# Performance work log

Hardware: AMD Instinct MI355X
Metric: run time of the kernel (lower is better)

## Reference

```python
import jax, jax.numpy as jnp
import numpy as np
import math

D_MODEL = 512
NUM_HEADS = 8
MAX_LEN = 10000.0


def positional_encoding_2d(seq_len, d_model, H, W, dtype=jnp.float32):
    # position along height repeated across width, and vice versa
    pos_h = jnp.repeat(jnp.arange(H, dtype=dtype), W)  # [H*W]
    pos_w = jnp.tile(jnp.arange(W, dtype=dtype), H)    # [H*W]
    div_term = jnp.exp(jnp.arange(0, d_model, 2, dtype=dtype) * (-(math.log(MAX_LEN) / d_model)))
    div = div_term[: d_model // 4]  # [d_model//4]
    pe = jnp.zeros((seq_len, d_model), dtype=dtype)
    pe = pe.at[:, 0::4].set(jnp.sin(pos_h[:, None] * div))
    pe = pe.at[:, 1::4].set(jnp.cos(pos_h[:, None] * div))
    pe = pe.at[:, 2::4].set(jnp.sin(pos_w[:, None] * div))
    pe = pe.at[:, 3::4].set(jnp.cos(pos_w[:, None] * div))
    return pe


def setup_inputs() -> dict:
    key = jax.random.key(0)
    ks = jax.random.split(key, 6)
    B, C, H, W = 8, D_MODEL, 32, 32
    d = D_MODEL
    s = 1.0 / math.sqrt(d)
    x = jax.random.normal(ks[0], (B, C, H, W), dtype=jnp.float32)
    Wq = jax.random.normal(ks[1], (d, d), dtype=jnp.float32) * s
    Wk = jax.random.normal(ks[2], (d, d), dtype=jnp.float32) * s
    Wv = jax.random.normal(ks[3], (d, d), dtype=jnp.float32) * s
    Wo = jax.random.normal(ks[4], (d, d), dtype=jnp.float32) * s
    bo = jnp.zeros((d,), dtype=jnp.float32)
    gamma = jnp.ones((d,), dtype=jnp.float32)
    beta = jnp.zeros((d,), dtype=jnp.float32)
    return {"x": x, "Wq": Wq, "Wk": Wk, "Wv": Wv, "Wo": Wo, "bo": bo, "gamma": gamma, "beta": beta}


def reference(x, Wq, Wk, Wv, Wo, bo, gamma, beta):
    B, C, H, W = x.shape
    d_model = C
    nh = NUM_HEADS
    dk = d_model // nh
    seq = H * W

    # [B, C, H, W] -> [B, seq, d_model]
    x_seq = x.reshape(B, C, seq).transpose(0, 2, 1)
    pe = positional_encoding_2d(seq, d_model, H, W, dtype=x.dtype)
    x_seq = x_seq + pe[None]
    residual = x_seq

    # QKV projections (torch Linear: y = x @ W.T)
    q = (x_seq @ Wq.T).reshape(B, seq, nh, dk).transpose(0, 2, 1, 3)  # [B, nh, S, dk]
    k = (x_seq @ Wk.T).reshape(B, seq, nh, dk).transpose(0, 2, 1, 3)
    v = (x_seq @ Wv.T).reshape(B, seq, nh, dk).transpose(0, 2, 1, 3)

    scores = jnp.einsum("bhsd,bhtd->bhst", q, k) / math.sqrt(dk)  # [B, nh, S, S]
    weights = jax.nn.softmax(scores, axis=-1)
    # dropout is identity at inference
    attn = jnp.einsum("bhst,bhtd->bhsd", weights, v)  # [B, nh, S, dk]
    attn = attn.transpose(0, 2, 1, 3).reshape(B, seq, d_model)

    out = attn @ Wo.T + bo
    y = out + residual
    mean = jnp.mean(y, axis=-1, keepdims=True)
    var = jnp.var(y, axis=-1, keepdims=True)
    y = (y - mean) / jnp.sqrt(var + 1e-5) * gamma + beta

    return y.transpose(0, 2, 1).reshape(B, C, H, W)
```

## Files before the change

kernel.cpp:

```cpp
#include <hip/hip_runtime.h>
#include <hip/hip_bf16.h>
#include <math.h>

#define DEV static __device__ __forceinline__

typedef unsigned short u16;
typedef unsigned int u32;
typedef __attribute__((ext_vector_type(4))) float f32x4;
typedef __attribute__((ext_vector_type(16))) float f32x16;
typedef __attribute__((ext_vector_type(8))) __bf16 bf16x8;
typedef __attribute__((ext_vector_type(4))) u16 u16x4;
typedef __attribute__((ext_vector_type(4))) u32 u32x4;

DEV u16 f2bf(float f) {
  unsigned u = __float_as_uint(f);
  u += 0x7fffu + ((u >> 16) & 1u);
  return (u16)(u >> 16);
}
DEV float bf2f(u16 x) { return __uint_as_float((u32)x << 16); }

DEV float fexp2(float x) { return __builtin_amdgcn_exp2f(x); }
DEV float fsin_rev(float rev) { return __builtin_amdgcn_sinf(rev); }
DEV float fcos_rev(float rev) { return __builtin_amdgcn_cosf(rev); }

DEV u32 cvt_pk_bf16(float lo, float hi) {
  u32 r;
  asm("v_cvt_pk_bf16_f32 %0, %1, %2" : "=v"(r) : "v"(lo), "v"(hi));
  return r;
}

DEV void perm32swap(u32& a, u32& b) {
  asm("v_permlane32_swap_b32 %0, %1" : "+v"(a), "+v"(b));
}

DEV void gl2lds16(const void* g, void* l) {
  __builtin_amdgcn_global_load_lds(
      (const __attribute__((address_space(1))) void*)g,
      (__attribute__((address_space(3))) void*)l, 16, 0, 0);
}

template<int RPW>
DEV void stage_rows(const u16* __restrict__ g, int gstride, u16* lds, int wave, int lane) {
  const int r_in = lane >> 3, slot = lane & 7;
  const int base_row = wave * RPW;
#pragma unroll
  for (int i = 0; i < RPW / 8; ++i) {
    const int row = base_row + i * 8 + r_in;
    const int sslot = slot ^ (row & 7);
    gl2lds16(g + (size_t)row * gstride + sslot * 8,
             lds + (size_t)(base_row + i * 8) * 64);
  }
}

DEV bf16x8 frag_read(const u16* lds, int row, int kslot) {
  const int slot = kslot ^ (row & 7);
  return *(const bf16x8*)(lds + row * 64 + slot * 8);
}

DEV f32x4 mfma16(bf16x8 a, bf16x8 b, f32x4 c) {
  return __builtin_amdgcn_mfma_f32_16x16x32_bf16(a, b, c, 0, 0, 0);
}
DEV f32x16 mfma32(bf16x8 a, bf16x8 b, f32x16 c) {
  return __builtin_amdgcn_mfma_f32_32x32x16_bf16(a, b, c, 0, 0, 0);
}

DEV size_t frag_elem(int row, int col) {
  return ((size_t)((row >> 4) * 16 + (col >> 5))) * 512
       + ((row & 15) + 16 * ((col >> 3) & 3)) * 8 + (col & 7);
}

__global__ __launch_bounds__(256) void pack_w(
    const float* __restrict__ w0, const float* __restrict__ w1,
    const float* __restrict__ w2, const float* __restrict__ w3,
    u16* __restrict__ dst) {
  const float* src = (blockIdx.y == 0) ? w0 : (blockIdx.y == 1) ? w1
                   : (blockIdx.y == 2) ? w2 : w3;
  const int lane = threadIdx.x & 63, wave = threadIdx.x >> 6;
  const int c16 = blockIdx.x >> 2;
  const int kchunk = (blockIdx.x & 3) * 4 + wave;
  const int cl = lane & 15, ko = lane >> 4;
  const float* s = src + (size_t)(c16 * 16 + cl) * 512 + kchunk * 32 + ko * 8;
  const f32x4 a = *(const f32x4*)(s);
  const f32x4 b = *(const f32x4*)(s + 4);
  u16x4 lo, hi;
#pragma unroll
  for (int j = 0; j < 4; ++j) { lo[j] = f2bf(a[j]); hi[j] = f2bf(b[j]); }
  u16* d = dst + (size_t)blockIdx.y * 262144
               + (size_t)(c16 * 16 + kchunk) * 512 + lane * 8;
  *(u16x4*)(d) = lo;
  *(u16x4*)(d + 4) = hi;
}

__global__ __launch_bounds__(256) void prep_x(
    const float* __restrict__ x, u16* __restrict__ Xa) {
  __shared__ float tile[32][33];
  const int b = blockIdx.z, c0 = blockIdx.y * 32, s0 = blockIdx.x * 32;
  const int t = threadIdx.x;
  const int cf = t >> 5, sf = t & 31;
#pragma unroll
  for (int i = 0; i < 4; ++i) {
    const int c = c0 + cf + i * 8;
    tile[cf + i * 8][sf] = x[((size_t)b * 512 + c) * 1024 + s0 + sf];
  }
  __syncthreads();
  const int cl = t & 31, sl = t >> 5;
  const int cg = c0 + cl;
  const int j = cg >> 2;
  const float dv = fexp2((float)j * -0.051905126482615f);
  const float dv_rev = dv * 0.15915494309189535f;
#pragma unroll
  for (int i = 0; i < 4; ++i) {
    const int s = s0 + sl + i * 8;
    const float pos = (cg & 2) ? (float)(s & 31) : (float)(s >> 5);
    float rev = pos * dv_rev;
    rev = rev - floorf(rev);
    const float pe = (cg & 1) ? fcos_rev(rev) : fsin_rev(rev);
    const float v = tile[cl][sl + i * 8] + pe;
    const int row = b * 1024 + s;
    Xa[frag_elem(row, cg)] = f2bf(v);
  }
}

__global__ __launch_bounds__(256) void gemm_qkv(
    const u16* __restrict__ Xa, const u16* __restrict__ Wpk,
    u16* __restrict__ Qb, u16* __restrict__ Kb, u16* __restrict__ Vtb,
    float qscale) {
  __shared__ __align__(16) u16 smem[128 * 132];
  const int t = threadIdx.x, lane = t & 63, wave = t >> 6;
  const int bn0 = blockIdx.x * 128, bm0 = blockIdx.y * 128;
  const int wr = wave >> 1, wc = wave & 1;
  const int colbase = bn0 + wc * 64;
  const int w = colbase >> 9;
  const int cb16 = (colbase & 511) >> 4;
  const u16* Bf = Wpk + (size_t)w * 262144;
  const int row16base = (bm0 >> 4) + wr * 4;
  f32x4 acc[4][4] = {};
#pragma unroll 4
  for (int kc = 0; kc < 16; ++kc) {
    bf16x8 af[4], bfr[4];
#pragma unroll
    for (int n = 0; n < 4; ++n)
      bfr[n] = *(const bf16x8*)(Bf + (size_t)((cb16 + n) * 16 + kc) * 512 + lane * 8);
#pragma unroll
    for (int m = 0; m < 4; ++m)
      af[m] = *(const bf16x8*)(Xa + (size_t)((row16base + m) * 16 + kc) * 512 + lane * 8);
#pragma unroll
    for (int m = 0; m < 4; ++m)
#pragma unroll
      for (int n = 0; n < 4; ++n)
        acc[m][n] = mfma16(af[m], bfr[n], acc[m][n]);
  }
  const int cl = lane & 15, rg = (lane >> 4) * 4;
  if (bn0 >= 1024) {
#pragma unroll
    for (int m = 0; m < 4; ++m)
#pragma unroll
      for (int n = 0; n < 4; ++n) {
        const int dvL = wc * 64 + n * 16 + cl;
        const int rowL0 = wr * 64 + m * 16 + rg;
        u16x4 pk;
#pragma unroll
        for (int r = 0; r < 4; ++r) pk[r] = f2bf(acc[m][n][r]);
        *(u16x4*)(smem + dvL * 132 + rowL0) = pk;
      }
    __syncthreads();
    const int dvg0 = bn0 - 1024;
#pragma unroll
    for (int i = 0; i < 16; ++i) {
      const int idx = i * 256 + t;
      const int dv = idx >> 5, ch = (idx & 31) * 4;
      const u16x4 v = *(const u16x4*)(smem + dv * 132 + ch);
      *(u16x4*)(Vtb + (size_t)(dvg0 + dv) * 8192 + bm0 + ch) = v;
    }
  } else {
    u16* dst = (bn0 >= 512) ? Kb : Qb;
    const float al = (bn0 >= 512) ? 1.0f : qscale;
    const int cb = (bn0 & 511) + wc * 64;
#pragma unroll
    for (int m = 0; m < 4; ++m)
#pragma unroll
      for (int n = 0; n < 4; ++n) {
        const int col = cb + n * 16 + cl;
#pragma unroll
        for (int r = 0; r < 4; ++r) {
          const int row = bm0 + wr * 64 + m * 16 + rg + r;
          dst[(size_t)row * 512 + col] = f2bf(acc[m][n][r] * al);
        }
      }
  }
}

__global__ __launch_bounds__(256) void gemm_ln(
    const u16* __restrict__ Obf, const u16* __restrict__ Wpk,
    const u16* __restrict__ Xa, const float* __restrict__ bias,
    const float* __restrict__ gamma, const float* __restrict__ beta,
    float* __restrict__ out) {
  __shared__ float fsm[4 * 128 * 33];
  __shared__ float redsum[4][32], redsq[4][32], srow[32][2];
  const int t = threadIdx.x, lane = t & 63, wave = t >> 6;
  const int m0 = blockIdx.x * 32;
  const int b = m0 >> 10, s0 = m0 & 1023;
  const int row16 = m0 >> 4;
  const u16* Bf = Wpk + (size_t)3 * 262144;
  f32x4 acc[2][8] = {};
#pragma unroll 4
  for (int kc = 0; kc < 16; ++kc) {
    bf16x8 af[2], bfr[8];
#pragma unroll
    for (int n = 0; n < 8; ++n)
      bfr[n] = *(const bf16x8*)(Bf + (size_t)((wave * 8 + n) * 16 + kc) * 512 + lane * 8);
#pragma unroll
    for (int m = 0; m < 2; ++m)
      af[m] = *(const bf16x8*)(Obf + (size_t)((row16 + m) * 16 + kc) * 512 + lane * 8);
#pragma unroll
    for (int m = 0; m < 2; ++m)
#pragma unroll
      for (int n = 0; n < 8; ++n)
        acc[m][n] = mfma16(af[m], bfr[n], acc[m][n]);
  }
  float* fw = fsm + wave * (128 * 33);
  const int cl = lane & 15, rg = (lane >> 4) * 4;
  float psum[8], psq[8];
#pragma unroll
  for (int i = 0; i < 8; ++i) { psum[i] = 0.f; psq[i] = 0.f; }
#pragma unroll
  for (int m = 0; m < 2; ++m)
#pragma unroll
    for (int n = 0; n < 8; ++n) {
      const int col_l = n * 16 + cl;
      const int col = wave * 128 + col_l;
      const float bi = bias[col];
#pragma unroll
      for (int r = 0; r < 4; ++r) {
        const int row_l = m * 16 + rg + r;
        const float v = acc[m][n][r] + bi
                      + bf2f(Xa[frag_elem(m0 + row_l, col)]);
        fw[col_l * 33 + row_l] = v;
        psum[m * 4 + r] += v;
        psq[m * 4 + r] += v * v;
      }
    }
#pragma unroll
  for (int i = 0; i < 8; ++i) {
#pragma unroll
    for (int off = 8; off >= 1; off >>= 1) {
      psum[i] += __shfl_xor(psum[i], off);
      psq[i]  += __shfl_xor(psq[i], off);
    }
  }
  if (cl == 0) {
#pragma unroll
    for (int m = 0; m < 2; ++m)
#pragma unroll
      for (int r = 0; r < 4; ++r) {
        const int row_l = m * 16 + rg + r;
        redsum[wave][row_l] = psum[m * 4 + r];
        redsq[wave][row_l]  = psq[m * 4 + r];
      }
  }
  __syncthreads();
  if (t < 32) {
    float s = redsum[0][t] + redsum[1][t] + redsum[2][t] + redsum[3][t];
    float q = redsq[0][t] + redsq[1][t] + redsq[2][t] + redsq[3][t];
    const float mean = s * (1.f / 512.f);
    const float var = q * (1.f / 512.f) - mean * mean;
    srow[t][0] = mean;
    srow[t][1] = rsqrtf(var + 1e-5f);
  }
  __syncthreads();
  const int row = lane & 31, chalf = lane >> 5;
  const float mean = srow[row][0], rstd = srow[row][1];
  float* outb = out + (size_t)b * 512 * 1024 + s0 + row;
#pragma unroll 4
  for (int cc = 0; cc < 64; ++cc) {
    const int col_l = cc * 2 + chalf;
    const int col = wave * 128 + col_l;
    const float v = (fw[col_l * 33 + row] - mean) * rstd;
    outb[(size_t)col * 1024] = v * gamma[col] + beta[col];
  }
}

__global__ __launch_bounds__(256, 2) void attn(
    const u16* __restrict__ Qb, const u16* __restrict__ Kb,
    const u16* __restrict__ Vt, u16* __restrict__ Obf) {
  __shared__ __align__(16) u16 Ks[2][64 * 64];
  __shared__ __align__(16) u16 Vs[2][64 * 64];
  const int t = threadIdx.x, lane = t & 63, wave = t >> 6;
  const int wg = blockIdx.x;
  const int b = wg & 7, h = (wg >> 3) & 7, qt = wg >> 6;
  const int qsub = wave & 1, half = wave >> 1;
  const int ql = lane & 31, hl = lane >> 5;
  const int q0 = qt * 64 + qsub * 32;
  bf16x8 bq[4];
  {
    const u16* qrow = Qb + ((size_t)b * 1024 + q0 + ql) * 512 + h * 64 + hl * 8;
#pragma unroll
    for (int c = 0; c < 4; ++c) bq[c] = *(const bf16x8*)(qrow + c * 16);
  }
  f32x16 ot[2] = {};
  float m_run = -1e30f, l_run = 0.f;
  u16* stg_dst = qsub ? Vs[half] : Ks[half];
  for (int i = 0; i < 8; ++i) {
    const int kb = half * 512 + i * 64;
    {
      const int r_in = lane >> 3, slot = lane & 7;
      const u16* src; size_t gs;
      if (qsub) { src = Vt + (size_t)(h * 64) * 8192 + (size_t)b * 1024 + kb; gs = 8192; }
      else      { src = Kb + ((size_t)b * 1024 + kb) * 512 + h * 64;          gs = 512; }
#pragma unroll
      for (int j = 0; j < 8; ++j) {
        const int row = j * 8 + r_in;
        const int ss = slot ^ (row & 7);
        gl2lds16(src + (size_t)row * gs + ss * 8, stg_dst + j * 512);
      }
    }
    __syncthreads();
    f32x16 st[2] = {};
    __builtin_amdgcn_s_setprio(1);
#pragma unroll
    for (int c = 0; c < 4; ++c) {
      bf16x8 a0 = frag_read(Ks[half], ql, c * 2 + hl);
      bf16x8 a1 = frag_read(Ks[half], 32 + ql, c * 2 + hl);
      st[0] = mfma32(a0, bq[c], st[0]);
      st[1] = mfma32(a1, bq[c], st[1]);
    }
    __builtin_amdgcn_s_setprio(0);
    float m0[8];
#pragma unroll
    for (int i2 = 0; i2 < 8; ++i2)
      m0[i2] = fmaxf(fmaxf(st[0][i2], st[0][i2 + 8]), fmaxf(st[1][i2], st[1][i2 + 8]));
#pragma unroll
    for (int i2 = 0; i2 < 4; ++i2) m0[i2] = fmaxf(m0[i2], m0[i2 + 4]);
    float mx = fmaxf(fmaxf(m0[0], m0[1]), fmaxf(m0[2], m0[3]));
    mx = fmaxf(mx, __shfl_xor(mx, 32));
    if (!__all(mx <= m_run + 8.f)) {
      const float mn = fmaxf(m_run, mx);
      const float sc = fexp2(m_run - mn);
      m_run = mn;
      l_run *= sc;
      ot[0] *= sc;
      ot[1] *= sc;
    }
#pragma unroll
    for (int i2 = 0; i2 < 16; ++i2) {
      st[0][i2] = fexp2(st[0][i2] - m_run);
      st[1][i2] = fexp2(st[1][i2] - m_run);
    }
    float s0[8];
#pragma unroll
    for (int i2 = 0; i2 < 8; ++i2)
      s0[i2] = (st[0][i2] + st[0][i2 + 8]) + (st[1][i2] + st[1][i2 + 8]);
#pragma unroll
    for (int i2 = 0; i2 < 4; ++i2) s0[i2] = s0[i2] + s0[i2 + 4];
    float rs = (s0[0] + s0[1]) + (s0[2] + s0[3]);
    rs += __shfl_xor(rs, 32);
    l_run += rs;
    __builtin_amdgcn_s_setprio(1);
#pragma unroll
    for (int c = 0; c < 4; ++c) {
      const int kf = c >> 1, i0 = (c & 1) * 4;
      u32 w0 = cvt_pk_bf16(st[kf][2 * i0 + 0], st[kf][2 * i0 + 1]);
      u32 w1 = cvt_pk_bf16(st[kf][2 * i0 + 2], st[kf][2 * i0 + 3]);
      u32 w2 = cvt_pk_bf16(st[kf][2 * i0 + 4], st[kf][2 * i0 + 5]);
      u32 w3 = cvt_pk_bf16(st[kf][2 * i0 + 6], st[kf][2 * i0 + 7]);
      perm32swap(w0, w2);
      perm32swap(w1, w3);
      u32x4 wv; wv.x = w0; wv.y = w1; wv.z = w2; wv.w = w3;
      bf16x8 bp = *(bf16x8*)&wv;
      bf16x8 v0 = frag_read(Vs[half], ql, c * 2 + hl);
      bf16x8 v1 = frag_read(Vs[half], 32 + ql, c * 2 + hl);
      ot[0] = mfma32(v0, bp, ot[0]);
      ot[1] = mfma32(v1, bp, ot[1]);
    }
    __builtin_amdgcn_s_setprio(0);
    __syncthreads();
  }
  float* Om = (float*)&Ks[0][0] + qsub * 2048;
  float* Ml = (float*)&Vs[0][0];
  if (wave >= 2) {
#pragma unroll
    for (int df = 0; df < 2; ++df)
#pragma unroll
      for (int r = 0; r < 16; ++r) {
        const int dr = (r & 3) + 8 * (r >> 2) + 4 * hl;
        Om[(df * 32 + dr) * 32 + ql] = ot[df][r];
      }
    if (hl == 0) {
      Ml[qsub * 64 + ql] = m_run;
      Ml[qsub * 64 + 32 + ql] = l_run;
    }
    __syncthreads();
  } else {
    __syncthreads();
    const float m2 = Ml[qsub * 64 + ql];
    const float l2 = Ml[qsub * 64 + 32 + ql];
    const float m = fmaxf(m_run, m2);
    const float a = fexp2(m_run - m);
    const float bsc = fexp2(m2 - m);
    const float inv = 1.f / (l_run * a + l2 * bsc);
    float v[2][16];
#pragma unroll
    for (int df = 0; df < 2; ++df)
#pragma unroll
      for (int r = 0; r < 16; ++r) {
        const int dr = (r & 3) + 8 * (r >> 2) + 4 * hl;
        v[df][r] = (ot[df][r] * a + Om[(df * 32 + dr) * 32 + ql] * bsc) * inv;
      }
    const int q = b * 1024 + q0 + ql;
#pragma unroll
    for (int p = 0; p < 4; ++p) {
      const int jjA = 2 * p, jjB = 2 * p + 1;
      const int dfA = jjA >> 2, rA = (jjA & 3) * 4;
      const int dfB = jjB >> 2, rB = (jjB & 3) * 4;
      u32 a0 = cvt_pk_bf16(v[dfA][rA + 0], v[dfA][rA + 1]);
      u32 a1 = cvt_pk_bf16(v[dfA][rA + 2], v[dfA][rA + 3]);
      u32 b0 = cvt_pk_bf16(v[dfB][rB + 0], v[dfB][rB + 1]);
      u32 b1 = cvt_pk_bf16(v[dfB][rB + 2], v[dfB][rB + 3]);
      perm32swap(a0, b0);
      perm32swap(a1, b1);
      const int jj = 2 * p + hl;
      const int d0 = h * 64 + jj * 8;
      u32x4 wv; wv.x = a0; wv.y = a1; wv.z = b0; wv.w = b1;
      u16* dst = Obf + ((size_t)((q >> 4) * 16 + (d0 >> 5))) * 512
                     + ((q & 15) + 16 * ((d0 >> 3) & 3)) * 8;
      *(u32x4*)dst = wv;
    }
  }
}

extern "C" void kernel_launch(void* const* d_in, const int* in_sizes, int n_in,
                              void* d_out, int out_size, void* d_ws, size_t ws_size,
                              hipStream_t stream) {
  const float* x     = (const float*)d_in[0];
  const float* Wq    = (const float*)d_in[1];
  const float* Wk    = (const float*)d_in[2];
  const float* Wv    = (const float*)d_in[3];
  const float* Wo    = (const float*)d_in[4];
  const float* bo    = (const float*)d_in[5];
  const float* gamma = (const float*)d_in[6];
  const float* beta  = (const float*)d_in[7];
  char* ws = (char*)d_ws;
  const size_t MB = 1048576;
  u16*   Xa    = (u16*)(ws);
  u16*   Wpk   = (u16*)(ws + 8 * MB);
  u16*   Qb    = (u16*)(ws + 10 * MB);
  u16*   Kb    = (u16*)(ws + 18 * MB);
  u16*   Vtb   = (u16*)(ws + 26 * MB);
  u16*   Obf   = (u16*)(ws + 34 * MB);

  pack_w<<<dim3(128, 4), 256, 0, stream>>>(Wq, Wk, Wv, Wo, Wpk);
  prep_x<<<dim3(32, 16, 8), 256, 0, stream>>>(x, Xa);
  gemm_qkv<<<dim3(12, 64), 256, 0, stream>>>(Xa, Wpk, Qb, Kb, Vtb,
                                             0.125f * 1.44269504088896f);
  attn<<<1024, 256, 0, stream>>>(Qb, Kb, Vtb, Obf);
  gemm_ln<<<256, 256, 0, stream>>>(Obf, Wpk, Xa, bo, gamma, beta,
                                   (float*)d_out);
}
```

Before: 95.95 us.

## Load K and V fragments directly from global memory in attention, dropping LDS staging

The attention kernel no longer stages K and V tiles into shared memory with async global-to-LDS copies and block barriers. Each wave now reads its MFMA operand fragments straight from global memory into registers, which removes the per-iteration __syncthreads and LDS traffic. The cost is that the two waves sharing a key range each fetch K and V themselves, raising global/L2 traffic. The V fragment reads use a large stride, and register pressure rises; the occupancy hint of 2 is also dropped from launch bounds.

Result: slower. 123.7 us (+29.0%).

```diff
diff --git a/kernel.cpp b/kernel.cpp
--- a/kernel.cpp
+++ b/kernel.cpp
@@ -31,30 +31,6 @@
 
 DEV void perm32swap(u32& a, u32& b) {
   asm("v_permlane32_swap_b32 %0, %1" : "+v"(a), "+v"(b));
-}
-
-DEV void gl2lds16(const void* g, void* l) {
-  __builtin_amdgcn_global_load_lds(
-      (const __attribute__((address_space(1))) void*)g,
-      (__attribute__((address_space(3))) void*)l, 16, 0, 0);
-}
-
-template<int RPW>
-DEV void stage_rows(const u16* __restrict__ g, int gstride, u16* lds, int wave, int lane) {
-  const int r_in = lane >> 3, slot = lane & 7;
-  const int base_row = wave * RPW;
-#pragma unroll
-  for (int i = 0; i < RPW / 8; ++i) {
-    const int row = base_row + i * 8 + r_in;
-    const int sslot = slot ^ (row & 7);
-    gl2lds16(g + (size_t)row * gstride + sslot * 8,
-             lds + (size_t)(base_row + i * 8) * 64);
-  }
-}
-
-DEV bf16x8 frag_read(const u16* lds, int row, int kslot) {
-  const int slot = kslot ^ (row & 7);
-  return *(const bf16x8*)(lds + row * 64 + slot * 8);
 }
 
 DEV f32x4 mfma16(bf16x8 a, bf16x8 b, f32x4 c) {
@@ -280,11 +256,11 @@
   }
 }
 
-__global__ __launch_bounds__(256, 2) void attn(
+__global__ __launch_bounds__(256) void attn(
     const u16* __restrict__ Qb, const u16* __restrict__ Kb,
     const u16* __restrict__ Vt, u16* __restrict__ Obf) {
-  __shared__ __align__(16) u16 Ks[2][64 * 64];
-  __shared__ __align__(16) u16 Vs[2][64 * 64];
+  __shared__ float OmS[2][2048];
+  __shared__ float MlS[128];
   const int t = threadIdx.x, lane = t & 63, wave = t >> 6;
   const int wg = blockIdx.x;
   const int b = wg & 7, h = (wg >> 3) & 7, qt = wg >> 6;
@@ -299,32 +275,31 @@
   }
   f32x16 ot[2] = {};
   float m_run = -1e30f, l_run = 0.f;
-  u16* stg_dst = qsub ? Vs[half] : Ks[half];
+  const u16* Kp0 = Kb + ((size_t)b * 1024 + half * 512) * 512 + h * 64;
+  const u16* Vp0 = Vt + ((size_t)(h * 64)) * 8192 + (size_t)b * 1024 + half * 512;
   for (int i = 0; i < 8; ++i) {
-    const int kb = half * 512 + i * 64;
-    {
-      const int r_in = lane >> 3, slot = lane & 7;
-      const u16* src; size_t gs;
-      if (qsub) { src = Vt + (size_t)(h * 64) * 8192 + (size_t)b * 1024 + kb; gs = 8192; }
-      else      { src = Kb + ((size_t)b * 1024 + kb) * 512 + h * 64;          gs = 512; }
-#pragma unroll
-      for (int j = 0; j < 8; ++j) {
-        const int row = j * 8 + r_in;
-        const int ss = slot ^ (row & 7);
-        gl2lds16(src + (size_t)row * gs + ss * 8, stg_dst + j * 512);
-      }
-    }
-    __syncthreads();
+    const u16* Kp = Kp0 + (size_t)i * 64 * 512;
+    const u16* Vp = Vp0 + i * 64;
+    bf16x8 k0[4], k1[4];
+#pragma unroll
+    for (int c = 0; c < 4; ++c) {
+      k0[c] = *(const bf16x8*)(Kp + (size_t)ql * 512 + (c * 2 + hl) * 8);
+      k1[c] = *(const bf16x8*)(Kp + (size_t)(32 + ql) * 512 + (c * 2 + hl) * 8);
+    }
     f32x16 st[2] = {};
     __builtin_amdgcn_s_setprio(1);
 #pragma unroll
     for (int c = 0; c < 4; ++c) {
-      bf16x8 a0 = frag_read(Ks[half], ql, c * 2 + hl);
-      bf16x8 a1 = frag_read(Ks[half], 32 + ql, c * 2 + hl);
-      st[0] = mfma32(a0, bq[c], st[0]);
-      st[1] = mfma32(a1, bq[c], st[1]);
+      st[0] = mfma32(k0[c], bq[c], st[0]);
+      st[1] = mfma32(k1[c], bq[c], st[1]);
     }
     __builtin_amdgcn_s_setprio(0);
+    bf16x8 v0[4], v1[4];
+#pragma unroll
+    for (int c = 0; c < 4; ++c) {
+      v0[c] = *(const bf16x8*)(Vp + (size_t)ql * 8192 + (c * 2 + hl) * 8);
+      v1[c] = *(const bf16x8*)(Vp + (size_t)(32 + ql) * 8192 + (c * 2 + hl) * 8);
+    }
     float m0[8];
 #pragma unroll
     for (int i2 = 0; i2 < 8; ++i2)
@@ -367,33 +342,28 @@
       perm32swap(w1, w3);
       u32x4 wv; wv.x = w0; wv.y = w1; wv.z = w2; wv.w = w3;
       bf16x8 bp = *(bf16x8*)&wv;
-      bf16x8 v0 = frag_read(Vs[half], ql, c * 2 + hl);
-      bf16x8 v1 = frag_read(Vs[half], 32 + ql, c * 2 + hl);
-      ot[0] = mfma32(v0, bp, ot[0]);
-      ot[1] = mfma32(v1, bp, ot[1]);
+      ot[0] = mfma32(v0[c], bp, ot[0]);
+      ot[1] = mfma32(v1[c], bp, ot[1]);
     }
     __builtin_amdgcn_s_setprio(0);
-    __syncthreads();
-  }
-  float* Om = (float*)&Ks[0][0] + qsub * 2048;
-  float* Ml = (float*)&Vs[0][0];
+  }
   if (wave >= 2) {
 #pragma unroll
     for (int df = 0; df < 2; ++df)
 #pragma unroll
       for (int r = 0; r < 16; ++r) {
         const int dr = (r & 3) + 8 * (r >> 2) + 4 * hl;
-        Om[(df * 32 + dr) * 32 + ql] = ot[df][r];
+        OmS[qsub][(df * 32 + dr) * 32 + ql] = ot[df][r];
       }
     if (hl == 0) {
-      Ml[qsub * 64 + ql] = m_run;
-      Ml[qsub * 64 + 32 + ql] = l_run;
+      MlS[qsub * 64 + ql] = m_run;
+      MlS[qsub * 64 + 32 + ql] = l_run;
     }
     __syncthreads();
   } else {
     __syncthreads();
-    const float m2 = Ml[qsub * 64 + ql];
-    const float l2 = Ml[qsub * 64 + 32 + ql];
+    const float m2 = MlS[qsub * 64 + ql];
+    const float l2 = MlS[qsub * 64 + 32 + ql];
     const float m = fmaxf(m_run, m2);
     const float a = fexp2(m_run - m);
     const float bsc = fexp2(m2 - m);
@@ -404,7 +374,7 @@
 #pragma unroll
       for (int r = 0; r < 16; ++r) {
         const int dr = (r & 3) + 8 * (r >> 2) + 4 * hl;
-        v[df][r] = (ot[df][r] * a + Om[(df * 32 + dr) * 32 + ql] * bsc) * inv;
+        v[df][r] = (ot[df][r] * a + OmS[qsub][(df * 32 + dr) * 32 + ql] * bsc) * inv;
       }
     const int q = b * 1024 + q0 + ql;
 #pragma unroll
```
